# Optimization experiments

Measured on AMD Instinct MI355X. Metric: run time of the kernel, lower is better.

## Reference

```python
import jax, jax.numpy as jnp
import numpy as np

B, A, U, S, E, H = 32768, 8, 64, 512, 128, 4
HYP = 256  # unused (two_hyper_layers=False)
COEF = 0.001
NEG = -99999999.0


def setup_inputs() -> dict:
    key = jax.random.key(0)
    ks = jax.random.split(key, 11)
    def lin(k, shape, fan_in):
        return jax.random.normal(k, shape, dtype=jnp.float32) * (1.0 / np.sqrt(fan_in))
    return {
        "agent_qs": jax.random.normal(ks[0], (B, A), dtype=jnp.float32),
        "states": jax.random.normal(ks[1], (B, S), dtype=jnp.float32),
        "actions": jax.random.randint(ks[2], (B, A), 0, 10, dtype=jnp.int64),
        "W_sel": lin(ks[3], (H, E, S), S),        # per-head selector extractor (no bias)
        "W_key": lin(ks[4], (H, E, U + 1), U + 1),  # per-head key extractor (no bias)
        "Wv1": lin(ks[5], (E, S), S),
        "bv1": jnp.zeros((E,), dtype=jnp.float32),
        "Wv2": lin(ks[6], (1, E), E),
        "bv2": jnp.zeros((1,), dtype=jnp.float32),
        "Wh": lin(ks[7], (H, S), S),              # hyper_w_head
        "bh": jnp.zeros((H,), dtype=jnp.float32),
    }


def reference(agent_qs, states, actions, W_sel, W_key, Wv1, bv1, Wv2, bv2, Wh, bh):
    b = states.shape[0]
    unit = states[:, : U * A].reshape(b, A, U)                     # [B,A,U]
    x = jnp.concatenate([unit, agent_qs[:, :, None]], axis=2)       # [B,A,U+1] (nonlinear)
    sel = jnp.einsum('bs,hes->bhe', states, W_sel)                  # all-head selectors
    keys = jnp.einsum('bau,heu->bhae', x, W_key)                    # all-head keys
    logits = jnp.einsum('bhe,bhae->bha', sel, keys)                 # attend_logits per head
    scaled = logits / np.float32(np.sqrt(E))
    dead = (actions == 0)[:, None, :]                               # mask_dead
    scaled = jnp.where(dead, NEG, scaled)
    weights = jax.nn.softmax(scaled, axis=2)                        # [B,H,A]
    v = jax.nn.relu(states @ Wv1.T + bv1) @ Wv2.T + bv2             # [B,1]
    w_head = jnp.abs(states @ Wh.T + bh)                            # [B,H] weighted_head
    head_attend = jnp.sum(weights * w_head[:, :, None], axis=1)     # [B,A]
    attend_mag_regs = COEF * jnp.sum(jnp.mean(logits ** 2, axis=(0, 2)))
    head_entropies = -jnp.mean(jnp.sum(jnp.log(weights + 1e-8) * weights, axis=2), axis=0)  # [H]
    return head_attend, v, attend_mag_regs, head_entropies
```

## Files before the change

### kernel.cpp

```cpp
#include <hip/hip_runtime.h>


typedef unsigned short u16;
typedef unsigned int u32;
typedef float f32x4 __attribute__((ext_vector_type(4)));
typedef unsigned int u32x4 __attribute__((ext_vector_type(4)));
typedef unsigned int u32x2 __attribute__((ext_vector_type(2)));
typedef __attribute__((address_space(1))) const u32 gu32;
typedef __attribute__((address_space(3))) u32 lu32;

#define NEGV -99999999.0f

__device__ __forceinline__ u16 f2bf(float f) {
  union { float f; u32 u; } v; v.f = f;
  u32 r = v.u + 0x7fffu + ((v.u >> 16) & 1u);
  return (u16)(r >> 16);
}
__device__ __forceinline__ float bfl(u32 w) { union { u32 u; float f; } v; v.u = w << 16; return v.f; }
__device__ __forceinline__ float bfh(u32 w) { union { u32 u; float f; } v; v.u = w & 0xffff0000u; return v.f; }

__global__ __launch_bounds__(256) void kprep(
    const float* __restrict__ Wsel, const float* __restrict__ Wkey,
    const float* __restrict__ Wv1, const float* __restrict__ Wh,
    u16* __restrict__ Wp, float* __restrict__ accs) {
  const int p = blockIdx.x;
  const int t = threadIdx.x;
  if (p == 0 && t < 16) accs[t] = 0.f;
#pragma unroll
  for (int half = 0; half < 2; ++half) {
    const int s = t + half * 256;
    float v = 0.f;
    if (p < 260) {
      int h, u;
      if (p < 256) { h = p >> 6; u = p & 63; } else { h = p - 256; u = 64; }
      const float* wk = Wkey + (size_t)h * 128 * 65 + u;
      const float* ws = Wsel + (size_t)h * 128 * 512 + s;
#pragma unroll 4
      for (int e = 0; e < 128; ++e) v = fmaf(wk[e * 65], ws[e * 512], v);
    } else if (p >= 264 && p < 392) {
      v = Wv1[(p - 264) * 512 + s];
    } else if (p >= 392 && p < 396) {
      v = Wh[(p - 392) * 512 + s];
    }
    const int kt = s >> 5, c = (s >> 3) & 3, j = s & 7;
    Wp[kt * 12800 + p * 32 + ((c ^ ((p >> 1) & 3)) << 3) + j] = f2bf(v);
  }
}

__device__ __forceinline__ void stageA(unsigned char* dst, const float4& x0, const float4& x1) {
  u32x4 aw;
  aw[0] = (u32)f2bf(x0.x) | ((u32)f2bf(x0.y) << 16);
  aw[1] = (u32)f2bf(x0.z) | ((u32)f2bf(x0.w) << 16);
  aw[2] = (u32)f2bf(x1.x) | ((u32)f2bf(x1.y) << 16);
  aw[3] = (u32)f2bf(x1.z) | ((u32)f2bf(x1.w) << 16);
  *(u32x4*)dst = aw;
}

__device__ __forceinline__ void stageB(unsigned char* ldsB, const char* gB, int wid) {
#pragma unroll
  for (int i = 0; i < 7; ++i) {
    const int c = wid + (i << 2);
    if (c < 25)
      __builtin_amdgcn_global_load_lds((gu32*)(gB + c * 1024),
                                       (lu32*)(ldsB + c * 1024), 16, 0, 0);
  }
}

__device__ __forceinline__ void computeT(const unsigned char* buf, int wid, int c16,
                                         int slot, f32x4 acc[4][7]) {
  u32x4 af[4];
#pragma unroll
  for (int r = 0; r < 4; ++r)
    af[r] = *(const u32x4*)(buf + (r * 16 + c16) * 64 + slot * 16);
#pragma unroll
  for (int i = 0; i < 7; ++i) {
    const int f = wid + (i << 2);
    if (f < 25) {
      u32x4 bfr = *(const u32x4*)(buf + 4096 + (f * 16 + c16) * 64 + slot * 16);
#pragma unroll
      for (int r = 0; r < 4; ++r)
        asm("v_mfma_f32_16x16x32_bf16 %0, %1, %2, %0"
            : "+v"(acc[r][i]) : "v"(af[r]), "v"(bfr));
    }
  }
}

__global__ __launch_bounds__(256, 2) void kmain(
    const float* __restrict__ states, const float* __restrict__ agent_qs,
    const int* __restrict__ actions, const u16* __restrict__ Wp,
    const float* __restrict__ bv1, const float* __restrict__ Wv2,
    const float* __restrict__ bv2, const float* __restrict__ bh,
    float* __restrict__ out, float* __restrict__ accs) {
  __shared__ __align__(16) unsigned char smem[59472];
  unsigned char* const buf0 = smem;
  unsigned char* const buf1 = smem + 29696;
  u16* const Ctile = (u16*)smem;
  float* const red = (float*)(smem + 59392);

  const int tid = threadIdx.x;
  const int wid = tid >> 6;
  const int lane = tid & 63;
  const int b0 = blockIdx.x * 64;

  const f32x4 zf = {0.f, 0.f, 0.f, 0.f};
  f32x4 acc[4][7];
#pragma unroll
  for (int r = 0; r < 4; ++r)
#pragma unroll
    for (int i = 0; i < 7; ++i) acc[r][i] = zf;

  const int ar = tid >> 2, ac = tid & 3;
  const float* aG = states + (size_t)(b0 + ar) * 512 + ac * 8;
  const int aWoff = ar * 64 + ((ac ^ ((ar >> 1) & 3)) << 4);

  const int c16 = lane & 15, sq = lane >> 4;
  const int slot = sq ^ ((c16 >> 1) & 3);
  const char* const wpB = (const char*)Wp + lane * 16;

  float4 ax = *(const float4*)(aG);
  float4 ay = *(const float4*)(aG + 4);
  stageA(buf0 + aWoff, ax, ay);
  stageB(buf0 + 4096, wpB, wid);
  ax = *(const float4*)(aG + 32);
  ay = *(const float4*)(aG + 36);
  __syncthreads();

  for (int kt = 0; kt < 14; ++kt) {
    unsigned char* const sb = (kt & 1) ? buf0 : buf1;
    unsigned char* const cb = (kt & 1) ? buf1 : buf0;
    stageA(sb + aWoff, ax, ay);
    stageB(sb + 4096, wpB + (size_t)(kt + 1) * 25600, wid);
    ax = *(const float4*)(aG + (kt + 2) * 32);
    ay = *(const float4*)(aG + (kt + 2) * 32 + 4);
    computeT(cb, wid, c16, slot, acc);
    __syncthreads();
  }
  stageA(buf1 + aWoff, ax, ay);
  stageB(buf1 + 4096, wpB + (size_t)15 * 25600, wid);
  computeT(buf0, wid, c16, slot, acc);
  __syncthreads();
  computeT(buf1, wid, c16, slot, acc);
  __syncthreads();

  asm volatile("s_nop 7\n\ts_nop 7" :::);

#pragma unroll
  for (int r = 0; r < 4; ++r)
#pragma unroll
    for (int i = 0; i < 7; ++i) {
      const int f = wid + (i << 2);
      if (f < 25) {
        const int col = (f << 4) + c16;
        const int rowb = (r << 4) + (sq << 2);
#pragma unroll
        for (int j = 0; j < 4; ++j)
          Ctile[(rowb + j) * 416 + col] = f2bf(acc[r][i][j]);
      }
    }
  __syncthreads();

  const int rloc = (wid << 4) + c16;
  const int b = b0 + rloc;
  const int qt = sq;
  const u16* crow = Ctile + rloc * 416;
  const float* srow = states + (size_t)b * 512;

  float m[4][16];
#pragma unroll
  for (int h = 0; h < 4; ++h) {
    u32x4 w0 = *(const u32x4*)(crow + h * 64 + qt * 16);
    u32x4 w1 = *(const u32x4*)(crow + h * 64 + qt * 16 + 8);
#pragma unroll
    for (int k = 0; k < 4; ++k) {
      m[h][2 * k] = bfl(w0[k]);     m[h][2 * k + 1] = bfh(w0[k]);
      m[h][8 + 2 * k] = bfl(w1[k]); m[h][8 + 2 * k + 1] = bfh(w1[k]);
    }
  }

  float lp[4][8];
#pragma unroll
  for (int h = 0; h < 4; ++h)
#pragma unroll
    for (int a = 0; a < 8; ++a) lp[h][a] = 0.f;

#pragma unroll
  for (int a = 0; a < 8; ++a) {
    const float* xp = srow + a * 64 + qt * 16;
    float4 v0 = *(const float4*)(xp);
    float4 v1 = *(const float4*)(xp + 4);
    float4 v2 = *(const float4*)(xp + 8);
    float4 v3 = *(const float4*)(xp + 12);
    float xv[16] = {v0.x, v0.y, v0.z, v0.w, v1.x, v1.y, v1.z, v1.w,
                    v2.x, v2.y, v2.z, v2.w, v3.x, v3.y, v3.z, v3.w};
#pragma unroll
    for (int h = 0; h < 4; ++h) {
      float s = 0.f;
#pragma unroll
      for (int t2 = 0; t2 < 16; ++t2) s = fmaf(m[h][t2], xv[t2], s);
      lp[h][a] += s;
    }
  }
#pragma unroll
  for (int h = 0; h < 4; ++h)
#pragma unroll
    for (int a = 0; a < 8; ++a) {
      float v = lp[h][a];
      v += __shfl_xor(v, 16, 64);
      v += __shfl_xor(v, 32, 64);
      lp[h][a] = v;
    }
  float4 q0 = *(const float4*)(agent_qs + (size_t)b * 8);
  float4 q1 = *(const float4*)(agent_qs + (size_t)b * 8 + 4);
  float qv[8] = {q0.x, q0.y, q0.z, q0.w, q1.x, q1.y, q1.z, q1.w};
  u32x2 w64 = *(const u32x2*)(crow + 256);
  float m64[4] = {bfl(w64[0]), bfh(w64[0]), bfl(w64[1]), bfh(w64[1])};
#pragma unroll
  for (int h = 0; h < 4; ++h)
#pragma unroll
    for (int a = 0; a < 8; ++a) lp[h][a] = fmaf(m64[h], qv[a], lp[h][a]);

  float magp = 0.f;
  if (qt == 0) {
#pragma unroll
    for (int h = 0; h < 4; ++h)
#pragma unroll
      for (int a = 0; a < 8; ++a) magp = fmaf(lp[h][a], lp[h][a], magp);
  }
  float bvv[32], wvv[32], cv[32];
#pragma unroll
  for (int g = 0; g < 8; ++g) {
    *(float4*)(bvv + g * 4) = *(const float4*)(bv1 + qt * 32 + g * 4);
    *(float4*)(wvv + g * 4) = *(const float4*)(Wv2 + qt * 32 + g * 4);
  }
#pragma unroll
  for (int g = 0; g < 4; ++g) {
    u32x4 wv = *(const u32x4*)(crow + 264 + qt * 32 + g * 8);
#pragma unroll
    for (int k = 0; k < 4; ++k) {
      cv[g * 8 + 2 * k] = bfl(wv[k]); cv[g * 8 + 2 * k + 1] = bfh(wv[k]);
    }
  }
  float vp = 0.f;
#pragma unroll
  for (int e2 = 0; e2 < 32; ++e2)
    vp = fmaf(fmaxf(cv[e2] + bvv[e2], 0.f), wvv[e2], vp);
  vp += __shfl_xor(vp, 16, 64);
  vp += __shfl_xor(vp, 32, 64);

  int av[8];
  const int* ap = actions + (size_t)b * 8;
#pragma unroll
  for (int a = 0; a < 8; ++a) av[a] = ap[a];

  u32x2 ww = *(const u32x2*)(crow + 392);
  float whr[4] = {bfl(ww[0]), bfh(ww[0]), bfl(ww[1]), bfh(ww[1])};
  float4 bh4 = *(const float4*)(bh);
  float bhv[4] = {bh4.x, bh4.y, bh4.z, bh4.w};

  const float scale = 0.088388347648318447f;
  float att[8];
#pragma unroll
  for (int a = 0; a < 8; ++a) att[a] = 0.f;
  float entp[4];
#pragma unroll
  for (int h = 0; h < 4; ++h) {
    float whv = fabsf(whr[h] + bhv[h]);
    float sc[8];
#pragma unroll
    for (int a = 0; a < 8; ++a)
      sc[a] = (av[a] == 0) ? NEGV : lp[h][a] * scale;
    float mx = sc[0];
#pragma unroll
    for (int a = 1; a < 8; ++a) mx = fmaxf(mx, sc[a]);
    float ex[8];
    float sum = 0.f;
#pragma unroll
    for (int a = 0; a < 8; ++a) { ex[a] = __expf(sc[a] - mx); sum += ex[a]; }
    float inv = 1.f / sum;
    float ent = 0.f;
#pragma unroll
    for (int a = 0; a < 8; ++a) {
      float w = ex[a] * inv;
      att[a] = fmaf(w, whv, att[a]);
      ent = fmaf(w, __logf(w + 1e-8f), ent);
    }
    entp[h] = ent;
  }

  if (qt == 0) {
    float4 o0 = {att[0], att[1], att[2], att[3]};
    float4 o1 = {att[4], att[5], att[6], att[7]};
    *(float4*)(out + (size_t)b * 8) = o0;
    *(float4*)(out + (size_t)b * 8 + 4) = o1;
    out[32768 * 8 + b] = vp + bv2[0];
  }

  float r0 = magp;
  float r1 = (qt == 0) ? entp[0] : 0.f;
  float r2 = (qt == 0) ? entp[1] : 0.f;
  float r3 = (qt == 0) ? entp[2] : 0.f;
  float r4 = (qt == 0) ? entp[3] : 0.f;
#pragma unroll
  for (int off = 1; off < 64; off <<= 1) {
    r0 += __shfl_xor(r0, off, 64);
    r1 += __shfl_xor(r1, off, 64);
    r2 += __shfl_xor(r2, off, 64);
    r3 += __shfl_xor(r3, off, 64);
    r4 += __shfl_xor(r4, off, 64);
  }
  if (lane == 0) {
    red[wid * 5 + 0] = r0; red[wid * 5 + 1] = r1; red[wid * 5 + 2] = r2;
    red[wid * 5 + 3] = r3; red[wid * 5 + 4] = r4;
  }
  __syncthreads();
  if (tid < 5) {
    float s = red[tid] + red[5 + tid] + red[10 + tid] + red[15 + tid];
    atomicAdd(&accs[tid], s);
  }
}

__global__ void kfin(const float* __restrict__ accs, float* __restrict__ out) {
  const int t = threadIdx.x;
  if (t == 0) out[294912] = 0.001f * accs[0] * (1.0f / 262144.0f);
  if (t >= 1 && t < 5) out[294912 + t] = -accs[t] * (1.0f / 32768.0f);
}

extern "C" void kernel_launch(void* const* d_in, const int* in_sizes, int n_in,
                              void* d_out, int out_size, void* d_ws, size_t ws_size,
                              hipStream_t stream) {
  const float* agent_qs = (const float*)d_in[0];
  const float* states   = (const float*)d_in[1];
  const int*   actions  = (const int*)d_in[2];
  const float* Wsel = (const float*)d_in[3];
  const float* Wkey = (const float*)d_in[4];
  const float* Wv1  = (const float*)d_in[5];
  const float* bv1  = (const float*)d_in[6];
  const float* Wv2  = (const float*)d_in[7];
  const float* bv2  = (const float*)d_in[8];
  const float* Wh   = (const float*)d_in[9];
  const float* bh   = (const float*)d_in[10];
  float* out = (float*)d_out;
  float* accs = (float*)d_ws;
  u16* Wp = (u16*)((char*)d_ws + 64);

  hipLaunchKernelGGL(kprep, dim3(400), dim3(256), 0, stream,
                     Wsel, Wkey, Wv1, Wh, Wp, accs);
  hipLaunchKernelGGL(kmain, dim3(512), dim3(256), 0, stream,
                     states, agent_qs, actions, Wp, bv1, Wv2, bv2, bh, out, accs);
  hipLaunchKernelGGL(kfin, dim3(1), dim3(64), 0, stream, accs, out);
}
```

Before: 59.69 us.

## Use 512-thread main blocks, tile weight-fold prep in LDS, fuse finalize via counter

The prep kernel now folds W_key into W_sel using LDS-staged tiles across 128 blocks instead of 400 blocks of strided global reads, with a separate small set of blocks copying Wv1/Wh. The main kernel doubles its block to 8 waves so each wave owns fewer output column tiles and accumulators, and the epilogue spreads each row over 8 lanes instead of 4. The final reduction kernel is replaced by a last-block-done atomic counter inside the main kernel, removing one launch. Risks include higher register and LDS pressure at 512 threads, the padded C-tile stride, and relying on the counter being zeroed by prep.

```diff
diff --git a/kernel.cpp b/kernel.cpp
--- a/kernel.cpp
+++ b/kernel.cpp
@@ -10,6 +10,7 @@
 typedef __attribute__((address_space(3))) u32 lu32;
 
 #define NEGV -99999999.0f
+#define CSTRIDE 424
 
 __device__ __forceinline__ u16 f2bf(float f) {
   union { float f; u32 u; } v; v.f = f;
@@ -19,62 +20,83 @@
 __device__ __forceinline__ float bfl(u32 w) { union { u32 u; float f; } v; v.u = w << 16; return v.f; }
 __device__ __forceinline__ float bfh(u32 w) { union { u32 u; float f; } v; v.u = w & 0xffff0000u; return v.f; }
 
+__device__ __forceinline__ void panel_store(u16* Wp, int p, int s, float v) {
+  const int kt = s >> 5, c = (s >> 3) & 3, j = s & 7;
+  Wp[kt * 12800 + p * 32 + ((c ^ ((p >> 1) & 3)) << 3) + j] = f2bf(v);
+}
+
 __global__ __launch_bounds__(256) void kprep(
     const float* __restrict__ Wsel, const float* __restrict__ Wkey,
     const float* __restrict__ Wv1, const float* __restrict__ Wh,
     u16* __restrict__ Wp, float* __restrict__ accs) {
-  const int p = blockIdx.x;
-  const int t = threadIdx.x;
-  if (p == 0 && t < 16) accs[t] = 0.f;
-#pragma unroll
-  for (int half = 0; half < 2; ++half) {
-    const int s = t + half * 256;
-    float v = 0.f;
-    if (p < 260) {
-      int h, u;
-      if (p < 256) { h = p >> 6; u = p & 63; } else { h = p - 256; u = 64; }
-      const float* wk = Wkey + (size_t)h * 128 * 65 + u;
-      const float* ws = Wsel + (size_t)h * 128 * 512 + s;
-#pragma unroll 4
-      for (int e = 0; e < 128; ++e) v = fmaf(wk[e * 65], ws[e * 512], v);
-    } else if (p >= 264 && p < 392) {
-      v = Wv1[(p - 264) * 512 + s];
-    } else if (p >= 392 && p < 396) {
-      v = Wh[(p - 392) * 512 + s];
-    }
-    const int kt = s >> 5, c = (s >> 3) & 3, j = s & 7;
-    Wp[kt * 12800 + p * 32 + ((c ^ ((p >> 1) & 3)) << 3) + j] = f2bf(v);
-  }
-}
-
-__device__ __forceinline__ void stageA(unsigned char* dst, const float4& x0, const float4& x1) {
-  u32x4 aw;
-  aw[0] = (u32)f2bf(x0.x) | ((u32)f2bf(x0.y) << 16);
-  aw[1] = (u32)f2bf(x0.z) | ((u32)f2bf(x0.w) << 16);
-  aw[2] = (u32)f2bf(x1.x) | ((u32)f2bf(x1.y) << 16);
-  aw[3] = (u32)f2bf(x1.z) | ((u32)f2bf(x1.w) << 16);
-  *(u32x4*)dst = aw;
+  const int bid = blockIdx.x, t = threadIdx.x;
+  if (bid < 128) {
+    __shared__ float wsS[2048];
+    __shared__ float wkS[8320];
+    const int h = bid >> 5, s0 = (bid & 31) << 4;
+    for (int i = t; i < 2048; i += 256)
+      wsS[i] = Wsel[((size_t)h * 128 + (i >> 4)) * 512 + s0 + (i & 15)];
+    for (int i = t; i < 8320; i += 256)
+      wkS[i] = Wkey[(size_t)h * 8320 + i];
+    __syncthreads();
+    {
+      const int u = t >> 2, sl0 = (t & 3) << 2;
+      float a0 = 0.f, a1 = 0.f, a2 = 0.f, a3 = 0.f;
+      for (int e = 0; e < 128; ++e) {
+        const float k = wkS[e * 65 + u];
+        const float* wr = wsS + e * 16 + sl0;
+        a0 = fmaf(k, wr[0], a0); a1 = fmaf(k, wr[1], a1);
+        a2 = fmaf(k, wr[2], a2); a3 = fmaf(k, wr[3], a3);
+      }
+      const int p = h * 64 + u, s = s0 + sl0;
+      panel_store(Wp, p, s, a0);     panel_store(Wp, p, s + 1, a1);
+      panel_store(Wp, p, s + 2, a2); panel_store(Wp, p, s + 3, a3);
+    }
+    if (t < 16) {
+      float a = 0.f;
+      for (int e = 0; e < 128; ++e)
+        a = fmaf(wkS[e * 65 + 64], wsS[e * 16 + t], a);
+      panel_store(Wp, 256 + h, s0 + t, a);
+    }
+  } else {
+    if (bid == 128 && t < 16) accs[t] = 0.f;
+    for (int row = 260 + (bid - 128); row < 400; row += 8) {
+      for (int s = t; s < 512; s += 256) {
+        float v = 0.f;
+        if (row >= 264 && row < 392) v = Wv1[(row - 264) * 512 + s];
+        else if (row >= 392 && row < 396) v = Wh[(row - 392) * 512 + s];
+        panel_store(Wp, row, s, v);
+      }
+    }
+  }
 }
 
 __device__ __forceinline__ void stageB(unsigned char* ldsB, const char* gB, int wid) {
 #pragma unroll
-  for (int i = 0; i < 7; ++i) {
-    const int c = wid + (i << 2);
+  for (int i = 0; i < 4; ++i) {
+    const int c = wid + (i << 3);
     if (c < 25)
       __builtin_amdgcn_global_load_lds((gu32*)(gB + c * 1024),
                                        (lu32*)(ldsB + c * 1024), 16, 0, 0);
   }
 }
 
+__device__ __forceinline__ void stageA8(unsigned char* dst, const float4& x) {
+  u32x2 w;
+  w[0] = (u32)f2bf(x.x) | ((u32)f2bf(x.y) << 16);
+  w[1] = (u32)f2bf(x.z) | ((u32)f2bf(x.w) << 16);
+  *(u32x2*)dst = w;
+}
+
 __device__ __forceinline__ void computeT(const unsigned char* buf, int wid, int c16,
-                                         int slot, f32x4 acc[4][7]) {
+                                         int slot, f32x4 acc[4][4]) {
   u32x4 af[4];
 #pragma unroll
   for (int r = 0; r < 4; ++r)
     af[r] = *(const u32x4*)(buf + (r * 16 + c16) * 64 + slot * 16);
 #pragma unroll
-  for (int i = 0; i < 7; ++i) {
-    const int f = wid + (i << 2);
+  for (int i = 0; i < 4; ++i) {
+    const int f = wid + (i << 3);
     if (f < 25) {
       u32x4 bfr = *(const u32x4*)(buf + 4096 + (f * 16 + c16) * 64 + slot * 16);
 #pragma unroll
@@ -85,13 +107,13 @@
   }
 }
 
-__global__ __launch_bounds__(256, 2) void kmain(
+__global__ __launch_bounds__(512, 4) void kmain(
     const float* __restrict__ states, const float* __restrict__ agent_qs,
     const int* __restrict__ actions, const u16* __restrict__ Wp,
     const float* __restrict__ bv1, const float* __restrict__ Wv2,
     const float* __restrict__ bv2, const float* __restrict__ bh,
     float* __restrict__ out, float* __restrict__ accs) {
-  __shared__ __align__(16) unsigned char smem[59472];
+  __shared__ __align__(16) unsigned char smem[59392 + 160];
   unsigned char* const buf0 = smem;
   unsigned char* const buf1 = smem + 29696;
   u16* const Ctile = (u16*)smem;
@@ -103,42 +125,35 @@
   const int b0 = blockIdx.x * 64;
 
   const f32x4 zf = {0.f, 0.f, 0.f, 0.f};
-  f32x4 acc[4][7];
+  f32x4 acc[4][4];
 #pragma unroll
   for (int r = 0; r < 4; ++r)
 #pragma unroll
-    for (int i = 0; i < 7; ++i) acc[r][i] = zf;
-
-  const int ar = tid >> 2, ac = tid & 3;
-  const float* aG = states + (size_t)(b0 + ar) * 512 + ac * 8;
-  const int aWoff = ar * 64 + ((ac ^ ((ar >> 1) & 3)) << 4);
+    for (int i = 0; i < 4; ++i) acc[r][i] = zf;
+
+  const int ar = tid >> 3, ac8 = tid & 7;
+  const float* aG = states + (size_t)(b0 + ar) * 512 + ac8 * 4;
+  const int aWoff = ar * 64 + (((ac8 >> 1) ^ ((ar >> 1) & 3)) << 4) + (ac8 & 1) * 8;
 
   const int c16 = lane & 15, sq = lane >> 4;
   const int slot = sq ^ ((c16 >> 1) & 3);
   const char* const wpB = (const char*)Wp + lane * 16;
 
   float4 ax = *(const float4*)(aG);
-  float4 ay = *(const float4*)(aG + 4);
-  stageA(buf0 + aWoff, ax, ay);
+  stageA8(buf0 + aWoff, ax);
   stageB(buf0 + 4096, wpB, wid);
   ax = *(const float4*)(aG + 32);
-  ay = *(const float4*)(aG + 36);
-  __syncthreads();
-
-  for (int kt = 0; kt < 14; ++kt) {
+  __syncthreads();
+
+  for (int kt = 0; kt < 15; ++kt) {
     unsigned char* const sb = (kt & 1) ? buf0 : buf1;
     unsigned char* const cb = (kt & 1) ? buf1 : buf0;
-    stageA(sb + aWoff, ax, ay);
+    stageA8(sb + aWoff, ax);
     stageB(sb + 4096, wpB + (size_t)(kt + 1) * 25600, wid);
-    ax = *(const float4*)(aG + (kt + 2) * 32);
-    ay = *(const float4*)(aG + (kt + 2) * 32 + 4);
+    if (kt < 14) ax = *(const float4*)(aG + (kt + 2) * 32);
     computeT(cb, wid, c16, slot, acc);
     __syncthreads();
   }
-  stageA(buf1 + aWoff, ax, ay);
-  stageB(buf1 + 4096, wpB + (size_t)15 * 25600, wid);
-  computeT(buf0, wid, c16, slot, acc);
-  __syncthreads();
   computeT(buf1, wid, c16, slot, acc);
   __syncthreads();
 
@@ -147,33 +162,31 @@
 #pragma unroll
   for (int r = 0; r < 4; ++r)
 #pragma unroll
-    for (int i = 0; i < 7; ++i) {
-      const int f = wid + (i << 2);
+    for (int i = 0; i < 4; ++i) {
+      const int f = wid + (i << 3);
       if (f < 25) {
         const int col = (f << 4) + c16;
         const int rowb = (r << 4) + (sq << 2);
 #pragma unroll
         for (int j = 0; j < 4; ++j)
-          Ctile[(rowb + j) * 416 + col] = f2bf(acc[r][i][j]);
+          Ctile[(rowb + j) * CSTRIDE + col] = f2bf(acc[r][i][j]);
       }
     }
   __syncthreads();
 
-  const int rloc = (wid << 4) + c16;
-  const int b = b0 + rloc;
-  const int qt = sq;
-  const u16* crow = Ctile + rloc * 416;
+  const int r = (wid << 3) + (lane >> 3);
+  const int q8 = lane & 7;
+  const int b = b0 + r;
+  const u16* crow = Ctile + r * CSTRIDE;
   const float* srow = states + (size_t)b * 512;
 
-  float m[4][16];
+  float m[4][8];
 #pragma unroll
   for (int h = 0; h < 4; ++h) {
-    u32x4 w0 = *(const u32x4*)(crow + h * 64 + qt * 16);
-    u32x4 w1 = *(const u32x4*)(crow + h * 64 + qt * 16 + 8);
+    u32x4 w = *(const u32x4*)(crow + h * 64 + q8 * 8);
 #pragma unroll
     for (int k = 0; k < 4; ++k) {
-      m[h][2 * k] = bfl(w0[k]);     m[h][2 * k + 1] = bfh(w0[k]);
-      m[h][8 + 2 * k] = bfl(w1[k]); m[h][8 + 2 * k + 1] = bfh(w1[k]);
+      m[h][2 * k] = bfl(w[k]); m[h][2 * k + 1] = bfh(w[k]);
     }
   }
 
@@ -185,19 +198,16 @@
 
 #pragma unroll
   for (int a = 0; a < 8; ++a) {
-    const float* xp = srow + a * 64 + qt * 16;
+    const float* xp = srow + a * 64 + q8 * 8;
     float4 v0 = *(const float4*)(xp);
     float4 v1 = *(const float4*)(xp + 4);
-    float4 v2 = *(const float4*)(xp + 8);
-    float4 v3 = *(const float4*)(xp + 12);
-    float xv[16] = {v0.x, v0.y, v0.z, v0.w, v1.x, v1.y, v1.z, v1.w,
-                    v2.x, v2.y, v2.z, v2.w, v3.x, v3.y, v3.z, v3.w};
+    float xv[8] = {v0.x, v0.y, v0.z, v0.w, v1.x, v1.y, v1.z, v1.w};
 #pragma unroll
     for (int h = 0; h < 4; ++h) {
       float s = 0.f;
 #pragma unroll
-      for (int t2 = 0; t2 < 16; ++t2) s = fmaf(m[h][t2], xv[t2], s);
-      lp[h][a] += s;
+      for (int j = 0; j < 8; ++j) s = fmaf(m[h][j], xv[j], s);
+      lp[h][a] = s;
     }
   }
 #pragma unroll
@@ -205,8 +215,9 @@
 #pragma unroll
     for (int a = 0; a < 8; ++a) {
       float v = lp[h][a];
-      v += __shfl_xor(v, 16, 64);
-      v += __shfl_xor(v, 32, 64);
+      v += __shfl_xor(v, 1, 64);
+      v += __shfl_xor(v, 2, 64);
+      v += __shfl_xor(v, 4, 64);
       lp[h][a] = v;
     }
   float4 q0 = *(const float4*)(agent_qs + (size_t)b * 8);
@@ -220,21 +231,21 @@
     for (int a = 0; a < 8; ++a) lp[h][a] = fmaf(m64[h], qv[a], lp[h][a]);
 
   float magp = 0.f;
-  if (qt == 0) {
+  if (q8 == 0) {
 #pragma unroll
     for (int h = 0; h < 4; ++h)
 #pragma unroll
       for (int a = 0; a < 8; ++a) magp = fmaf(lp[h][a], lp[h][a], magp);
   }
-  float bvv[32], wvv[32], cv[32];
-#pragma unroll
-  for (int g = 0; g < 8; ++g) {
-    *(float4*)(bvv + g * 4) = *(const float4*)(bv1 + qt * 32 + g * 4);
-    *(float4*)(wvv + g * 4) = *(const float4*)(Wv2 + qt * 32 + g * 4);
-  }
+  float bvv[16], wvv[16], cv[16];
 #pragma unroll
   for (int g = 0; g < 4; ++g) {
-    u32x4 wv = *(const u32x4*)(crow + 264 + qt * 32 + g * 8);
+    *(float4*)(bvv + g * 4) = *(const float4*)(bv1 + q8 * 16 + g * 4);
+    *(float4*)(wvv + g * 4) = *(const float4*)(Wv2 + q8 * 16 + g * 4);
+  }
+#pragma unroll
+  for (int g = 0; g < 2; ++g) {
+    u32x4 wv = *(const u32x4*)(crow + 264 + q8 * 16 + g * 8);
 #pragma unroll
     for (int k = 0; k < 4; ++k) {
       cv[g * 8 + 2 * k] = bfl(wv[k]); cv[g * 8 + 2 * k + 1] = bfh(wv[k]);
@@ -242,10 +253,11 @@
   }
   float vp = 0.f;
 #pragma unroll
-  for (int e2 = 0; e2 < 32; ++e2)
+  for (int e2 = 0; e2 < 16; ++e2)
     vp = fmaf(fmaxf(cv[e2] + bvv[e2], 0.f), wvv[e2], vp);
-  vp += __shfl_xor(vp, 16, 64);
-  vp += __shfl_xor(vp, 32, 64);
+  vp += __shfl_xor(vp, 1, 64);
+  vp += __shfl_xor(vp, 2, 64);
+  vp += __shfl_xor(vp, 4, 64);
 
   int av[8];
   const int* ap = actions + (size_t)b * 8;
@@ -287,19 +299,19 @@
     entp[h] = ent;
   }
 
-  if (qt == 0) {
+  if (q8 == 0) {
     float4 o0 = {att[0], att[1], att[2], att[3]};
     float4 o1 = {att[4], att[5], att[6], att[7]};
     *(float4*)(out + (size_t)b * 8) = o0;
     *(float4*)(out + (size_t)b * 8 + 4) = o1;
-    out[32768 * 8 + b] = vp + bv2[0];
+    out[262144 + b] = vp + bv2[0];
   }
 
   float r0 = magp;
-  float r1 = (qt == 0) ? entp[0] : 0.f;
-  float r2 = (qt == 0) ? entp[1] : 0.f;
-  float r3 = (qt == 0) ? entp[2] : 0.f;
-  float r4 = (qt == 0) ? entp[3] : 0.f;
+  float r1 = (q8 == 0) ? entp[0] : 0.f;
+  float r2 = (q8 == 0) ? entp[1] : 0.f;
+  float r3 = (q8 == 0) ? entp[2] : 0.f;
+  float r4 = (q8 == 0) ? entp[3] : 0.f;
 #pragma unroll
   for (int off = 1; off < 64; off <<= 1) {
     r0 += __shfl_xor(r0, off, 64);
@@ -314,15 +326,27 @@
   }
   __syncthreads();
   if (tid < 5) {
-    float s = red[tid] + red[5 + tid] + red[10 + tid] + red[15 + tid];
+    float s = 0.f;
+#pragma unroll
+    for (int w = 0; w < 8; ++w) s += red[w * 5 + tid];
     atomicAdd(&accs[tid], s);
   }
-}
-
-__global__ void kfin(const float* __restrict__ accs, float* __restrict__ out) {
-  const int t = threadIdx.x;
-  if (t == 0) out[294912] = 0.001f * accs[0] * (1.0f / 262144.0f);
-  if (t >= 1 && t < 5) out[294912 + t] = -accs[t] * (1.0f / 32768.0f);
+  __syncthreads();
+  if (tid == 0) {
+    u32* cnt = (u32*)(accs + 8);
+    if (atomicAdd(cnt, 1u) == 511u) {
+      float a0 = atomicAdd(&accs[0], 0.f);
+      float a1 = atomicAdd(&accs[1], 0.f);
+      float a2 = atomicAdd(&accs[2], 0.f);
+      float a3 = atomicAdd(&accs[3], 0.f);
+      float a4 = atomicAdd(&accs[4], 0.f);
+      out[294912] = 0.001f * a0 * (1.0f / 262144.0f);
+      out[294913] = -a1 * (1.0f / 32768.0f);
+      out[294914] = -a2 * (1.0f / 32768.0f);
+      out[294915] = -a3 * (1.0f / 32768.0f);
+      out[294916] = -a4 * (1.0f / 32768.0f);
+    }
+  }
 }
 
 extern "C" void kernel_launch(void* const* d_in, const int* in_sizes, int n_in,
@@ -343,9 +367,8 @@
   float* accs = (float*)d_ws;
   u16* Wp = (u16*)((char*)d_ws + 64);
 
-  hipLaunchKernelGGL(kprep, dim3(400), dim3(256), 0, stream,
+  hipLaunchKernelGGL(kprep, dim3(136), dim3(256), 0, stream,
                      Wsel, Wkey, Wv1, Wh, Wp, accs);
-  hipLaunchKernelGGL(kmain, dim3(512), dim3(256), 0, stream,
+  hipLaunchKernelGGL(kmain, dim3(512), dim3(512), 0, stream,
                      states, agent_qs, actions, Wp, bv1, Wv2, bv2, bh, out, accs);
-  hipLaunchKernelGGL(kfin, dim3(1), dim3(64), 0, stream, accs, out);
-}
+}
```

New measurement: 56.41 us. 5.5% less time.

## Load weight fragments directly from global, restructure prep kernel, fold finalize into main

Applied to the files above, without the earlier changes.

The prep kernel now computes the fused selector-key weight product with LDS tiling across 136 blocks, replacing 400 blocks that each re-read global memory with strided access. The main kernel stops staging B panels into LDS and has each lane read its MFMA B fragment straight from global, relying on caching. This shrinks shared memory, and occupancy is raised to 3 blocks per CU. The separate finalize kernel is replaced by a last-block-done atomic counter, and the C tile stride is padded to avoid bank conflicts. The risks are higher global and cache latency on the B loads inside the MFMA loop, and relying on the counter in accs being reset each call.

```diff
diff --git a/kernel.cpp b/kernel.cpp
--- a/kernel.cpp
+++ b/kernel.cpp
@@ -4,12 +4,12 @@
 typedef unsigned short u16;
 typedef unsigned int u32;
 typedef float f32x4 __attribute__((ext_vector_type(4)));
+typedef short s16x8 __attribute__((ext_vector_type(8)));
 typedef unsigned int u32x4 __attribute__((ext_vector_type(4)));
 typedef unsigned int u32x2 __attribute__((ext_vector_type(2)));
-typedef __attribute__((address_space(1))) const u32 gu32;
-typedef __attribute__((address_space(3))) u32 lu32;
 
 #define NEGV -99999999.0f
+#define CSTRIDE 424
 
 __device__ __forceinline__ u16 f2bf(float f) {
   union { float f; u32 u; } v; v.f = f;
@@ -19,31 +19,53 @@
 __device__ __forceinline__ float bfl(u32 w) { union { u32 u; float f; } v; v.u = w << 16; return v.f; }
 __device__ __forceinline__ float bfh(u32 w) { union { u32 u; float f; } v; v.u = w & 0xffff0000u; return v.f; }
 
+__device__ __forceinline__ void panel_store(u16* Wp, int p, int s, float v) {
+  Wp[(s >> 5) * 12800 + p * 32 + (s & 31)] = f2bf(v);
+}
+
 __global__ __launch_bounds__(256) void kprep(
     const float* __restrict__ Wsel, const float* __restrict__ Wkey,
     const float* __restrict__ Wv1, const float* __restrict__ Wh,
     u16* __restrict__ Wp, float* __restrict__ accs) {
-  const int p = blockIdx.x;
-  const int t = threadIdx.x;
-  if (p == 0 && t < 16) accs[t] = 0.f;
-#pragma unroll
-  for (int half = 0; half < 2; ++half) {
-    const int s = t + half * 256;
-    float v = 0.f;
-    if (p < 260) {
-      int h, u;
-      if (p < 256) { h = p >> 6; u = p & 63; } else { h = p - 256; u = 64; }
-      const float* wk = Wkey + (size_t)h * 128 * 65 + u;
-      const float* ws = Wsel + (size_t)h * 128 * 512 + s;
-#pragma unroll 4
-      for (int e = 0; e < 128; ++e) v = fmaf(wk[e * 65], ws[e * 512], v);
-    } else if (p >= 264 && p < 392) {
-      v = Wv1[(p - 264) * 512 + s];
-    } else if (p >= 392 && p < 396) {
-      v = Wh[(p - 392) * 512 + s];
-    }
-    const int kt = s >> 5, c = (s >> 3) & 3, j = s & 7;
-    Wp[kt * 12800 + p * 32 + ((c ^ ((p >> 1) & 3)) << 3) + j] = f2bf(v);
+  const int bid = blockIdx.x, t = threadIdx.x;
+  if (bid < 128) {
+    __shared__ float wsS[2048];
+    __shared__ float wkS[8320];
+    const int h = bid >> 5, s0 = (bid & 31) << 4;
+    for (int i = t; i < 2048; i += 256)
+      wsS[i] = Wsel[((size_t)h * 128 + (i >> 4)) * 512 + s0 + (i & 15)];
+    for (int i = t; i < 8320; i += 256)
+      wkS[i] = Wkey[(size_t)h * 8320 + i];
+    __syncthreads();
+    {
+      const int u = t >> 2, sl0 = (t & 3) << 2;
+      float a0 = 0.f, a1 = 0.f, a2 = 0.f, a3 = 0.f;
+      for (int e = 0; e < 128; ++e) {
+        const float k = wkS[e * 65 + u];
+        const float* wr = wsS + e * 16 + sl0;
+        a0 = fmaf(k, wr[0], a0); a1 = fmaf(k, wr[1], a1);
+        a2 = fmaf(k, wr[2], a2); a3 = fmaf(k, wr[3], a3);
+      }
+      const int p = h * 64 + u, s = s0 + sl0;
+      panel_store(Wp, p, s, a0);     panel_store(Wp, p, s + 1, a1);
+      panel_store(Wp, p, s + 2, a2); panel_store(Wp, p, s + 3, a3);
+    }
+    if (t < 16) {
+      float a = 0.f;
+      for (int e = 0; e < 128; ++e)
+        a = fmaf(wkS[e * 65 + 64], wsS[e * 16 + t], a);
+      panel_store(Wp, 256 + h, s0 + t, a);
+    }
+  } else {
+    if (bid == 128 && t < 16) accs[t] = 0.f;
+    for (int row = 260 + (bid - 128); row < 400; row += 8) {
+      for (int s = t; s < 512; s += 256) {
+        float v = 0.f;
+        if (row >= 264 && row < 392) v = Wv1[(row - 264) * 512 + s];
+        else if (row >= 392 && row < 396) v = Wh[(row - 392) * 512 + s];
+        panel_store(Wp, row, s, v);
+      }
+    }
   }
 }
 
@@ -56,50 +78,43 @@
   *(u32x4*)dst = aw;
 }
 
-__device__ __forceinline__ void stageB(unsigned char* ldsB, const char* gB, int wid) {
-#pragma unroll
-  for (int i = 0; i < 7; ++i) {
-    const int c = wid + (i << 2);
-    if (c < 25)
-      __builtin_amdgcn_global_load_lds((gu32*)(gB + c * 1024),
-                                       (lu32*)(ldsB + c * 1024), 16, 0, 0);
-  }
-}
-
-__device__ __forceinline__ void computeT(const unsigned char* buf, int wid, int c16,
-                                         int slot, f32x4 acc[4][7]) {
-  u32x4 af[4];
+__device__ __forceinline__ void computeT(const unsigned char* buf, int kt,
+                                         const u16* const bQ[7], int wid,
+                                         int c16, int slot, f32x4 acc[4][7]) {
+  s16x8 af[4];
 #pragma unroll
   for (int r = 0; r < 4; ++r)
-    af[r] = *(const u32x4*)(buf + (r * 16 + c16) * 64 + slot * 16);
+    af[r] = *(const s16x8*)(buf + (r * 16 + c16) * 64 + slot * 16);
 #pragma unroll
   for (int i = 0; i < 7; ++i) {
     const int f = wid + (i << 2);
     if (f < 25) {
-      u32x4 bfr = *(const u32x4*)(buf + 4096 + (f * 16 + c16) * 64 + slot * 16);
+      s16x8 bfr = *(const s16x8*)(bQ[i] + kt * 12800);
 #pragma unroll
       for (int r = 0; r < 4; ++r)
-        asm("v_mfma_f32_16x16x32_bf16 %0, %1, %2, %0"
-            : "+v"(acc[r][i]) : "v"(af[r]), "v"(bfr));
-    }
-  }
-}
-
-__global__ __launch_bounds__(256, 2) void kmain(
+        acc[r][i] = __builtin_amdgcn_mfma_f32_16x16x32_bf16(
+            af[r], bfr, acc[r][i], 0, 0, 0);
+    }
+  }
+}
+
+__global__ __launch_bounds__(256, 3) void kmain(
     const float* __restrict__ states, const float* __restrict__ agent_qs,
     const int* __restrict__ actions, const u16* __restrict__ Wp,
     const float* __restrict__ bv1, const float* __restrict__ Wv2,
     const float* __restrict__ bv2, const float* __restrict__ bh,
     float* __restrict__ out, float* __restrict__ accs) {
-  __shared__ __align__(16) unsigned char smem[59472];
+  __shared__ __align__(16) unsigned char smem[54272 + 80];
   unsigned char* const buf0 = smem;
-  unsigned char* const buf1 = smem + 29696;
+  unsigned char* const buf1 = smem + 4096;
   u16* const Ctile = (u16*)smem;
-  float* const red = (float*)(smem + 59392);
+  float* const red = (float*)(smem + 54272);
 
   const int tid = threadIdx.x;
   const int wid = tid >> 6;
   const int lane = tid & 63;
+  const int c16 = lane & 15, sq = lane >> 4;
+  const int slot = sq ^ ((c16 >> 1) & 3);
   const int b0 = blockIdx.x * 64;
 
   const f32x4 zf = {0.f, 0.f, 0.f, 0.f};
@@ -113,36 +128,34 @@
   const float* aG = states + (size_t)(b0 + ar) * 512 + ac * 8;
   const int aWoff = ar * 64 + ((ac ^ ((ar >> 1) & 3)) << 4);
 
-  const int c16 = lane & 15, sq = lane >> 4;
-  const int slot = sq ^ ((c16 >> 1) & 3);
-  const char* const wpB = (const char*)Wp + lane * 16;
+  const u16* bQ[7];
+#pragma unroll
+  for (int i = 0; i < 7; ++i) {
+    const int f = wid + (i << 2);
+    bQ[i] = Wp + ((f < 25 ? f : 0) * 16 + c16) * 32 + sq * 8;
+  }
 
   float4 ax = *(const float4*)(aG);
   float4 ay = *(const float4*)(aG + 4);
   stageA(buf0 + aWoff, ax, ay);
-  stageB(buf0 + 4096, wpB, wid);
   ax = *(const float4*)(aG + 32);
   ay = *(const float4*)(aG + 36);
   __syncthreads();
 
-  for (int kt = 0; kt < 14; ++kt) {
+#pragma unroll 2
+  for (int kt = 0; kt < 15; ++kt) {
     unsigned char* const sb = (kt & 1) ? buf0 : buf1;
     unsigned char* const cb = (kt & 1) ? buf1 : buf0;
     stageA(sb + aWoff, ax, ay);
-    stageB(sb + 4096, wpB + (size_t)(kt + 1) * 25600, wid);
-    ax = *(const float4*)(aG + (kt + 2) * 32);
-    ay = *(const float4*)(aG + (kt + 2) * 32 + 4);
-    computeT(cb, wid, c16, slot, acc);
+    if (kt < 14) {
+      ax = *(const float4*)(aG + (kt + 2) * 32);
+      ay = *(const float4*)(aG + (kt + 2) * 32 + 4);
+    }
+    computeT(cb, kt, bQ, wid, c16, slot, acc);
     __syncthreads();
   }
-  stageA(buf1 + aWoff, ax, ay);
-  stageB(buf1 + 4096, wpB + (size_t)15 * 25600, wid);
-  computeT(buf0, wid, c16, slot, acc);
-  __syncthreads();
-  computeT(buf1, wid, c16, slot, acc);
-  __syncthreads();
-
-  asm volatile("s_nop 7\n\ts_nop 7" :::);
+  computeT(buf1, 15, bQ, wid, c16, slot, acc);
+  __syncthreads();
 
 #pragma unroll
   for (int r = 0; r < 4; ++r)
@@ -154,7 +167,7 @@
         const int rowb = (r << 4) + (sq << 2);
 #pragma unroll
         for (int j = 0; j < 4; ++j)
-          Ctile[(rowb + j) * 416 + col] = f2bf(acc[r][i][j]);
+          Ctile[(rowb + j) * CSTRIDE + col] = f2bf(acc[r][i][j]);
       }
     }
   __syncthreads();
@@ -162,7 +175,7 @@
   const int rloc = (wid << 4) + c16;
   const int b = b0 + rloc;
   const int qt = sq;
-  const u16* crow = Ctile + rloc * 416;
+  const u16* crow = Ctile + rloc * CSTRIDE;
   const float* srow = states + (size_t)b * 512;
 
   float m[4][16];
@@ -292,7 +305,7 @@
     float4 o1 = {att[4], att[5], att[6], att[7]};
     *(float4*)(out + (size_t)b * 8) = o0;
     *(float4*)(out + (size_t)b * 8 + 4) = o1;
-    out[32768 * 8 + b] = vp + bv2[0];
+    out[262144 + b] = vp + bv2[0];
   }
 
   float r0 = magp;
@@ -317,12 +330,22 @@
     float s = red[tid] + red[5 + tid] + red[10 + tid] + red[15 + tid];
     atomicAdd(&accs[tid], s);
   }
-}
-
-__global__ void kfin(const float* __restrict__ accs, float* __restrict__ out) {
-  const int t = threadIdx.x;
-  if (t == 0) out[294912] = 0.001f * accs[0] * (1.0f / 262144.0f);
-  if (t >= 1 && t < 5) out[294912 + t] = -accs[t] * (1.0f / 32768.0f);
+  __syncthreads();
+  if (tid == 0) {
+    u32* cnt = (u32*)(accs + 8);
+    if (atomicAdd(cnt, 1u) == 511u) {
+      float a0 = atomicAdd(&accs[0], 0.f);
+      float a1 = atomicAdd(&accs[1], 0.f);
+      float a2 = atomicAdd(&accs[2], 0.f);
+      float a3 = atomicAdd(&accs[3], 0.f);
+      float a4 = atomicAdd(&accs[4], 0.f);
+      out[294912] = 0.001f * a0 * (1.0f / 262144.0f);
+      out[294913] = -a1 * (1.0f / 32768.0f);
+      out[294914] = -a2 * (1.0f / 32768.0f);
+      out[294915] = -a3 * (1.0f / 32768.0f);
+      out[294916] = -a4 * (1.0f / 32768.0f);
+    }
+  }
 }
 
 extern "C" void kernel_launch(void* const* d_in, const int* in_sizes, int n_in,
@@ -343,9 +366,8 @@
   float* accs = (float*)d_ws;
   u16* Wp = (u16*)((char*)d_ws + 64);
 
-  hipLaunchKernelGGL(kprep, dim3(400), dim3(256), 0, stream,
+  hipLaunchKernelGGL(kprep, dim3(136), dim3(256), 0, stream,
                      Wsel, Wkey, Wv1, Wh, Wp, accs);
   hipLaunchKernelGGL(kmain, dim3(512), dim3(256), 0, stream,
                      states, agent_qs, actions, Wp, bv1, Wv2, bv2, bh, out, accs);
-  hipLaunchKernelGGL(kfin, dim3(1), dim3(64), 0, stream, accs, out);
-}
+}
```

Result: slower. 109.7 us (+83.8%).
